# Performance work log

Hardware: AMD Instinct MI355X
Metric: run time of the kernel (lower is better)

Reference implementation:

```python
import jax, jax.numpy as jnp
import numpy as np

N_QUBITS = 14
N_LAYERS = 4
N_CLASSES = 10
BATCH = 1024


def apply_1q(state, gate, wire):
    """Apply a 2x2 gate ([2,2] shared or [B,2,2] batched) to `wire` of state [B,2,...,2]."""
    s = jnp.moveaxis(state, wire + 1, -1)
    shp = s.shape
    s = s.reshape(shp[0], -1, 2)
    if gate.ndim == 3:
        s = jnp.einsum('bij,bkj->bki', gate, s)
    else:
        s = jnp.einsum('ij,bkj->bki', gate, s)
    return jnp.moveaxis(s.reshape(shp), -1, wire + 1)


def apply_cnot(state, c, t):
    s = jnp.moveaxis(state, (c + 1, t + 1), (-2, -1))
    s = jnp.stack([s[..., 0, :], s[..., 1, ::-1]], axis=-2)
    return jnp.moveaxis(s, (-2, -1), (c + 1, t + 1))


def simulate(x, q_params):
    """Batched statevector sim of: RY(x_i) embed -> BasicEntanglerLayers(RX + CNOT ring) -> <Z_i>."""
    B, n = x.shape
    state = jnp.zeros((B,) + (2,) * n, jnp.complex64)
    state = state.at[(slice(None),) + (0,) * n].set(1.0)

    # RY(x_i) on each wire (angles batched per sample)
    c, s = jnp.cos(0.5 * x), jnp.sin(0.5 * x)
    for w in range(n):
        g = jnp.stack([jnp.stack([c[:, w], -s[:, w]], -1),
                       jnp.stack([s[:, w], c[:, w]], -1)], -2).astype(jnp.complex64)  # [B,2,2]
        state = apply_1q(state, g, w)

    # BasicEntanglerLayers: per layer RX(weights[l,i]) on every wire, then CNOT ring
    cw, sw = jnp.cos(0.5 * q_params), jnp.sin(0.5 * q_params)
    n_layers = q_params.shape[0]
    for l in range(n_layers):
        for w in range(n):
            cc = cw[l, w].astype(jnp.complex64)
            isw = (-1j) * sw[l, w].astype(jnp.complex64)
            g = jnp.stack([jnp.stack([cc, isw]), jnp.stack([isw, cc])])  # [2,2] RX
            state = apply_1q(state, g, w)
        if n == 2:
            state = apply_cnot(state, 0, 1)
        else:
            for w in range(n):
                state = apply_cnot(state, w, (w + 1) % n)

    # <Z_i> = P(bit_i=0) - P(bit_i=1)
    p = jnp.abs(state) ** 2  # [B,2,...,2] real
    axes_all = tuple(range(1, n + 1))
    z = []
    for w in range(n):
        pw = jnp.sum(p, axis=tuple(a for a in axes_all if a != w + 1))  # [B,2]
        z.append(pw[:, 0] - pw[:, 1])
    return jnp.stack(z, -1).astype(jnp.float32)  # [B, n]


def setup_inputs() -> dict:
    key = jax.random.key(0)
    k1, k2, k3, k4 = jax.random.split(key, 4)
    x = jax.random.normal(k1, (BATCH, N_QUBITS), dtype=jnp.float32)
    q_params = 0.01 * jax.random.normal(k2, (N_LAYERS, N_QUBITS), dtype=jnp.float32)
    fc_w = jax.random.normal(k3, (N_CLASSES, N_QUBITS), dtype=jnp.float32) / np.sqrt(N_QUBITS)
    fc_b = jax.random.normal(k4, (N_CLASSES,), dtype=jnp.float32) * 0.01
    return {"x": x, "q_params": q_params, "fc_w": fc_w, "fc_b": fc_b}


def reference(x, q_params, fc_w, fc_b):
    q_out = simulate(x, q_params)            # [B, n_qubits]
    logits = q_out @ fc_w.T + fc_b           # [B, n_classes]
    return logits
```

## Files before the change

kernel.cpp:

```cpp
#include <hip/hip_runtime.h>
#include <hip/hip_fp16.h>
#include <math.h>


#define NQ 14
#define NLAYERS 4
#define NCLASSES 10
#define BLOCK 512

typedef _Float16 f16;
typedef _Float16 f16x2 __attribute__((ext_vector_type(2)));
typedef _Float16 f16x4 __attribute__((ext_vector_type(4)));
typedef _Float16 f16x8 __attribute__((ext_vector_type(8)));
typedef float f32x4 __attribute__((ext_vector_type(4)));
typedef unsigned int u32;
typedef u32 u32x2 __attribute__((ext_vector_type(2)));

__device__ __forceinline__ f32x4 mf(f16x8 a, f16x8 b, f32x4 c) {
  return __builtin_amdgcn_mfma_f32_16x16x32_f16(a, b, c, 0, 0, 0);
}
__device__ __forceinline__ f32x4 mf16(f16x4 a, f16x4 b, f32x4 c) {
  return __builtin_amdgcn_mfma_f32_16x16x16f16(a, b, c, 0, 0, 0);
}
__device__ __forceinline__ int swz(int t) { return ((t ^ (t >> 3)) & 7) << 3; }

__device__ __forceinline__ f16x4 cvt4(f32x4 v) {
  u32x2 r;
  r[0] = __builtin_bit_cast(u32, __builtin_amdgcn_cvt_pkrtz(v[0], v[1]));
  r[1] = __builtin_bit_cast(u32, __builtin_amdgcn_cvt_pkrtz(v[2], v[3]));
  return __builtin_bit_cast(f16x4, r);
}
__device__ __forceinline__ u32 dwof(f16x4 v, int k) {
  return __builtin_bit_cast(u32x2, v)[k];
}

__device__ __forceinline__ int finv5(int n) {
  n ^= ((n >> 3) & 1) << 4;
  n ^= ((n >> 2) & 1) << 3;
  n ^= ((n >> 1) & 1) << 2;
  n ^= (n & 1) << 1;
  return n;
}
__device__ __forceinline__ int finv3(int n) {
  n ^= ((n >> 2) & 1) << 3;
  n ^= ((n >> 1) & 1) << 2;
  n ^= (n & 1) << 1;
  return n;
}

__global__ void qsim_build(const float* __restrict__ qp,
                           f16* __restrict__ gB, f16* __restrict__ gC) {
  __shared__ float qc[NLAYERS * NQ], qs[NLAYERS * NQ];
  const int tid = threadIdx.x;
  if (tid < NLAYERS * NQ) {
    float sv, cv; sincosf(0.5f * qp[tid], &sv, &cv);
    qc[tid] = cv; qs[tid] = sv;
  }
  __syncthreads();
#pragma unroll
  for (int p = 0; p < 7; ++p) {
    const int l = (p + 1) >> 1;
    const int base = 14 * l + ((p & 1) ? 0 : 5);
    const float c0 = qc[base], c1 = qc[base+1], c2 = qc[base+2], c3 = qc[base+3], c4 = qc[base+4];
    const float s0 = qs[base], s1 = qs[base+1], s2 = qs[base+2], s3 = qs[base+3], s4 = qs[base+4];
#pragma unroll
    for (int e = tid; e < 1024; e += BLOCK) {
      const int n = e >> 5, k = e & 31;
      const int d = finv5(n) ^ k;
      float mag = ((d & 1) ? s0 : c0) * ((d & 2) ? s1 : c1);
      mag *= ((d & 4) ? s2 : c2) * ((d & 8) ? s3 : c3);
      mag *= ((d & 16) ? s4 : c4);
      const int t = __popc(d) & 3;
      const f16 v = (f16)((t == 1 || t == 2) ? -mag : mag);
      const int pp = 256 * (k >> 3) + 8 * n + (k & 7);
      const bool isreal = !(t & 1);
      gB[p * 2048 + pp]        = isreal ? v : (f16)0.f;
      gB[p * 2048 + pp + 1024] = isreal ? (f16)0.f : v;
    }
  }
#pragma unroll
  for (int e = tid; e < 1024; e += BLOCK) {
    const int li = e >> 8, rp = (e >> 4) & 15, k = e & 15;
    const int base = 14 * li + 10;
    const float c0 = qc[base], c1 = qc[base+1], c2 = qc[base+2], c3 = qc[base+3];
    const float s0 = qs[base], s1 = qs[base+1], s2 = qs[base+2], s3 = qs[base+3];
    const int d = finv3(rp) ^ k;
    float mag = ((d & 1) ? s0 : c0) * ((d & 2) ? s1 : c1);
    mag *= ((d & 4) ? s2 : c2) * ((d & 8) ? s3 : c3);
    const int t = __popc(d) & 3;
    const f16 v = (f16)((t == 1 || t == 2) ? -mag : mag);
    const bool isreal = !(t & 1);
    const int pp = li * 512 + 16 * rp + k;
    gC[pp]       = isreal ? v : (f16)0.f;
    gC[pp + 256] = isreal ? (f16)0.f : v;
  }
}

struct FB { f16x8 br0, bi0, br1, bi1; };
struct FC { f16x4 ur0, ui0, ur1, ui1; };

__device__ __forceinline__ FB loadB(const f16* __restrict__ g, bool ctrl, int tid) {
  const int lane = tid & 63, wave = tid >> 6;
  const int q = lane >> 4, cc = lane & 15;
  int n0 = cc, n1 = cc | 16;
  if (ctrl && wave >= 4) { n0 ^= 31; n1 ^= 31; }
  FB f;
  f.br0 = *(const f16x8*)(g + 256 * q + 8 * n0);
  f.bi0 = *(const f16x8*)(g + 1024 + 256 * q + 8 * n0);
  f.br1 = *(const f16x8*)(g + 256 * q + 8 * n1);
  f.bi1 = *(const f16x8*)(g + 1024 + 256 * q + 8 * n1);
  return f;
}
__device__ __forceinline__ FC loadC(const f16* __restrict__ g, int tid) {
  const int lane = tid & 63;
  const int q = lane >> 4, cc = lane & 15;
  const int r0 = 16 * cc + 4 * q, r1 = 16 * (cc ^ 15) + 4 * q;
  FC f;
  f.ur0 = *(const f16x4*)(g + r0);
  f.ui0 = *(const f16x4*)(g + 256 + r0);
  f.ur1 = *(const f16x4*)(g + r1);
  f.ui1 = *(const f16x4*)(g + 256 + r1);
  return f;
}

__device__ __forceinline__ void passA(f16* __restrict__ reP, f16* __restrict__ imP,
                                      const FB fb,
                                      const f16* __restrict__ gNB,
                                      const f16* __restrict__ gNC,
                                      FB* __restrict__ nextB,
                                      FC* __restrict__ nextC, int tid) {
  const int lane = tid & 63, wave = tid >> 6;
  const int q = lane >> 4, cc = lane & 15;
  f16x8 Ar[4], Ai[4];
#pragma unroll
  for (int i = 0; i < 4; ++i) {
    const int mt = wave * 4 + i;
    const int pA = mt * 512 + ((128 * q + 8 * cc) ^ swz(mt));
    Ar[i] = *(const f16x8*)(reP + pA);
    Ai[i] = *(const f16x8*)(imP + pA);
  }
  __syncthreads();
  *nextB = loadB(gNB, true, tid);
  *nextC = loadC(gNC, tid);
  f16x4 outR[8], outI[8];
#pragma unroll
  for (int i = 0; i < 4; ++i) {
    const f16x8 nAi = -Ai[i];
    {
      f32x4 aR = {0.f,0.f,0.f,0.f}, aI = {0.f,0.f,0.f,0.f};
      aR = mf(Ar[i], fb.br0, aR); aR = mf(nAi, fb.bi0, aR);
      aI = mf(Ar[i], fb.bi0, aI); aI = mf(Ai[i], fb.br0, aI);
      outR[i * 2 + 0] = cvt4(aR);
      outI[i * 2 + 0] = cvt4(aI);
    }
    {
      f32x4 aR = {0.f,0.f,0.f,0.f}, aI = {0.f,0.f,0.f,0.f};
      aR = mf(Ar[i], fb.br1, aR); aR = mf(nAi, fb.bi1, aR);
      aI = mf(Ar[i], fb.bi1, aI); aI = mf(Ai[i], fb.br1, aI);
      outR[i * 2 + 1] = cvt4(aR);
      outI[i * 2 + 1] = cvt4(aI);
    }
  }
#pragma unroll
  for (int i = 0; i < 4; ++i) {
    const int mt = wave * 4 + i;
#pragma unroll
    for (int nt = 0; nt < 2; ++nt) {
      const int n5 = nt * 16 + cc;
      const int pS = n5 * 512 +
          ((128 * (2 * (mt & 1) + (q >> 1)) + 8 * (mt >> 1) + 4 * (q & 1)) ^ swz(n5));
      *(f16x4*)(reP + pS) = outR[i * 2 + nt];
      *(f16x4*)(imP + pS) = outI[i * 2 + nt];
    }
  }
}

template<bool FINAL>
__device__ __forceinline__ void superBC(f16* __restrict__ reP, f16* __restrict__ imP,
                                        const FB fb, const FC fc,
                                        const f16* __restrict__ gNB,
                                        FB* __restrict__ nextB,
                                        int tid, float* __restrict__ zloc) {
  const int lane = tid & 63, wave = tid >> 6;
  const int q = lane >> 4, cc = lane & 15;
  f16x8 Ar[4], Ai[4];
#pragma unroll
  for (int i = 0; i < 4; ++i) {
    const int mt = wave * 4 + i;
    const int pA = mt * 512 + ((128 * q + 8 * cc) ^ swz(mt));
    Ar[i] = *(const f16x8*)(reP + pA);
    Ai[i] = *(const f16x8*)(imP + pA);
  }
  if constexpr (!FINAL) {
    __syncthreads();
    *nextB = loadB(gNB, false, tid);
  }
  const f16x4 ucn0 = -fc.ui0, ucn1 = -fc.ui1;

  f16x4 accR[4][2], accI[4][2];
  float z0b = 0.f, z1b = 0.f, z9b = 0.f, zA = 0.f, zB = 0.f, pt = 0.f;
#pragma unroll
  for (int i = 0; i < 4; ++i) {
    const f16x8 nAi = -Ai[i];
#pragma unroll
    for (int h = 0; h < 2; ++h) {
      const f16x8 br = h ? fb.br1 : fb.br0;
      const f16x8 bi = h ? fb.bi1 : fb.bi0;
      f32x4 aR = {0.f,0.f,0.f,0.f}, aI = {0.f,0.f,0.f,0.f};
      aR = mf(Ar[i], br, aR); aR = mf(nAi, bi, aR);
      aI = mf(Ar[i], bi, aI); aI = mf(Ai[i], br, aI);
      const f16x4 s1r = cvt4(aR), s1i = cvt4(aI);
      const f16x4 ur = h ? fc.ur1 : fc.ur0;
      const f16x4 ui = h ? fc.ui1 : fc.ui0;
      const f16x4 un = h ? ucn1 : ucn0;
      f32x4 cR = {0.f,0.f,0.f,0.f}, cI = {0.f,0.f,0.f,0.f};
      cR = mf16(ur, s1r, cR); cR = mf16(un, s1i, cR);
      cI = mf16(ui, s1r, cI); cI = mf16(ur, s1i, cI);
      if constexpr (FINAL) {
        const float p0 = cR[0]*cR[0] + cI[0]*cI[0];
        const float p1 = cR[1]*cR[1] + cI[1]*cI[1];
        const float p2 = cR[2]*cR[2] + cI[2]*cI[2];
        const float p3 = cR[3]*cR[3] + cI[3]*cI[3];
        const float ps = (p0 + p1) + (p2 + p3);
        zA += (p0 - p1) + (p2 - p3);
        zB += (p0 + p1) - (p2 + p3);
        z0b += (i & 1) ? -ps : ps;
        z1b += (i & 2) ? -ps : ps;
        z9b += h ? -ps : ps;
        pt  += ps;
      } else {
        accR[i][h] = cvt4(cR);
        accI[i][h] = cvt4(cI);
      }
    }
  }
  if constexpr (FINAL) {
    zloc[0]  += (q & 2) ? -z0b : z0b;
    zloc[1]  += z1b;
    zloc[2]  += (wave & 1) ? -pt : pt;
    zloc[3]  += (wave & 2) ? -pt : pt;
    zloc[4]  += (wave & 4) ? -pt : pt;
    zloc[5]  += (cc & 1) ? -pt : pt;
    zloc[6]  += (cc & 2) ? -pt : pt;
    zloc[7]  += (cc & 4) ? -pt : pt;
    zloc[8]  += (cc & 8) ? -pt : pt;
    zloc[9]  += z9b;
    zloc[10] += zA;
    zloc[11] += zB;
    zloc[12] += (q & 1) ? -pt : pt;
    zloc[13] += (q & 2) ? -pt : pt;
  } else {
    const u32 selLo = (q & 2) ? 0x01000504u : 0x05040100u;
    const u32 selHi = (q & 2) ? 0x03020706u : 0x07060302u;
    const int ibase = 128 * (wave >> 1) + 4 * (wave & 1);
#pragma unroll
    for (int h = 0; h < 2; ++h) {
#pragma unroll
      for (int j = 0; j < 4; ++j) {
        const int pS = (8 * q + 2 * j + h) * 512 + ibase +
                       8 * (cc ^ (2 * j + h) ^ q);
        const int dj = j >> 1;
        const u32 sel = (j & 1) ? selHi : selLo;
        u32x2 vr, vi;
        vr[0] = __builtin_amdgcn_perm(dwof(accR[1][h], dj), dwof(accR[0][h], dj), sel);
        vr[1] = __builtin_amdgcn_perm(dwof(accR[3][h], dj), dwof(accR[2][h], dj), sel);
        vi[0] = __builtin_amdgcn_perm(dwof(accI[1][h], dj), dwof(accI[0][h], dj), sel);
        vi[1] = __builtin_amdgcn_perm(dwof(accI[3][h], dj), dwof(accI[2][h], dj), sel);
        *(u32x2*)(reP + pS) = vr;
        *(u32x2*)(imP + pS) = vi;
      }
    }
  }
}

__global__ __launch_bounds__(BLOCK, 4) void qsim_kernel(
    const float* __restrict__ x, const float* __restrict__ qp,
    const float* __restrict__ fcw, const float* __restrict__ fcb,
    const f16* __restrict__ gB, const f16* __restrict__ gC,
    float* __restrict__ out) {
  extern __shared__ unsigned char smem[];
  f16* reP = (f16*)smem;
  f16* imP = reP + 16384;
  float* scratch = (float*)(imP + 16384);
  float* qc = scratch + 128;
  float* qs = qc + 8;
  float* xc = qs + 8;
  float* xs = xc + 16;

  const int b = blockIdx.x;
  const int tid = threadIdx.x;

  FB fb = loadB(gB, true, tid);
  FC fc = loadC(gC, tid);

  if (tid < NQ) {
    float sv, cv; sincosf(0.5f * x[b * NQ + tid], &sv, &cv);
    xc[tid] = cv; xs[tid] = sv;
  } else if (tid >= 64 && tid < 64 + 5) {
    const int k = tid - 64;
    float sv, cv; sincosf(0.5f * qp[k], &sv, &cv);
    qc[k] = cv; qs[k] = sv;
  }
  __syncthreads();

  float* Flo  = scratch;
  float* psi  = Flo + 32;
  float* PsiR = psi + 32;
  float* PsiI = PsiR + 32;
  if (tid < 32) {
    float f = 1.f;
#pragma unroll
    for (int j = 0; j < 5; ++j) f *= ((tid >> j) & 1) ? xs[5 + j] : xc[5 + j];
    Flo[tid] = f;
  } else if (tid < 64) {
    const int k = tid - 32;
    float f = 1.f;
#pragma unroll
    for (int j = 0; j < 5; ++j) f *= ((k >> j) & 1) ? xs[j] : xc[j];
    psi[k] = f;
  }
  __syncthreads();
  if (tid < 32) {
    const float c0 = qc[0], c1 = qc[1], c2 = qc[2], c3 = qc[3], c4 = qc[4];
    const float s0 = qs[0], s1 = qs[1], s2 = qs[2], s3 = qs[3], s4 = qs[4];
    const int a = finv5(tid);
    float ar = 0.f, ai = 0.f;
    for (int k = 0; k < 32; ++k) {
      const int d = a ^ k;
      float mag = ((d & 1) ? s0 : c0) * ((d & 2) ? s1 : c1);
      mag *= ((d & 4) ? s2 : c2) * ((d & 8) ? s3 : c3);
      mag *= ((d & 16) ? s4 : c4);
      mag *= psi[k];
      const int t = __popc(d) & 3;
      if (t == 0) ar += mag; else if (t == 1) ai -= mag;
      else if (t == 2) ar -= mag; else ai += mag;
    }
    PsiR[tid] = ar; PsiI[tid] = ai;
  }
  __syncthreads();
  {
    float fhi = 1.f;
#pragma unroll
    for (int j = 0; j < 4; ++j) fhi *= ((tid >> j) & 1) ? xs[10 + j] : xc[10 + j];
    const float cr = fhi * PsiR[tid >> 4], ci = fhi * PsiI[tid >> 4];
    const int t = tid >> 4;
    const int sz = swz(t);
#pragma unroll
    for (int kb = 0; kb < 4; ++kb) {
      f16x8 hr, hi;
#pragma unroll
      for (int j = 0; j < 8; ++j) {
        const float F = Flo[8 * kb + j];
        hr[j] = (f16)(F * cr);
        hi[j] = (f16)(F * ci);
      }
      const int pb = t * 512 + ((128 * kb + 8 * (tid & 15)) ^ sz);
      *(f16x8*)(reP + pb) = hr;
      *(f16x8*)(imP + pb) = hi;
    }
  }
  __syncthreads();

  FB fbN; FC fcN;
  superBC<false>(reP, imP, fb, fc, gB + 1 * 2048, &fbN, tid, nullptr);
  __syncthreads();
#pragma unroll
  for (int l = 1; l < NLAYERS; ++l) {
    passA(reP, imP, fbN, gB + (2 * l) * 2048, gC + l * 512, &fb, &fc, tid);
    __syncthreads();
    if (l < NLAYERS - 1) {
      superBC<false>(reP, imP, fb, fc, gB + (2 * l + 1) * 2048, &fbN, tid, nullptr);
      __syncthreads();
    }
  }

  float zloc[NQ];
#pragma unroll
  for (int w = 0; w < NQ; ++w) zloc[w] = 0.f;
  superBC<true>(reP, imP, fb, fc, nullptr, nullptr, tid, zloc);
  __syncthreads();

  float* zpart = scratch;
  float* zbuf  = zpart + 112;
#pragma unroll
  for (int w = 0; w < NQ; ++w) {
#pragma unroll
    for (int off = 32; off > 0; off >>= 1)
      zloc[w] += __shfl_down(zloc[w], off, 64);
  }
  const int wave = tid >> 6, lane = tid & 63;
  if (lane == 0) {
#pragma unroll
    for (int w = 0; w < NQ; ++w) zpart[wave * NQ + w] = zloc[w];
  }
  __syncthreads();
  if (tid < NQ) {
    float a = 0.f;
#pragma unroll
    for (int v = 0; v < 8; ++v) a += zpart[v * NQ + tid];
    zbuf[tid] = a;
  }
  __syncthreads();
  if (tid < NCLASSES) {
    float acc = fcb[tid];
#pragma unroll
    for (int w = 0; w < NQ; ++w) acc = fmaf(zbuf[w], fcw[tid * NQ + w], acc);
    out[b * NCLASSES + tid] = acc;
  }
}

extern "C" void kernel_launch(void* const* d_in, const int* in_sizes, int n_in,
                              void* d_out, int out_size, void* d_ws, size_t ws_size,
                              hipStream_t stream) {
  const float* x   = (const float*)d_in[0];
  const float* qp  = (const float*)d_in[1];
  const float* fcw = (const float*)d_in[2];
  const float* fcb = (const float*)d_in[3];
  float* out = (float*)d_out;
  const int B = in_sizes[0] / NQ;

  f16* gB = (f16*)d_ws;
  f16* gC = gB + 7 * 2048;

  qsim_build<<<1, BLOCK, 0, stream>>>(qp, gB, gC);

  const size_t shmem = (size_t)(2 * 16384) * sizeof(f16)
                     + (size_t)(128 + 8 + 8 + 16 + 16) * sizeof(float);
  (void)hipFuncSetAttribute((const void*)qsim_kernel,
                            hipFuncAttributeMaxDynamicSharedMemorySize, (int)shmem);
  qsim_kernel<<<B, BLOCK, shmem, stream>>>(x, qp, fcw, fcb, gB, gC, out);
}
```

Before: 119.5 us.

## Halve LDS staging by exchanging real and imaginary parts sequentially through one buffer

The state is now held in registers between passes, and only one 32KB LDS staging buffer is used. Real and imaginary parts are transposed through it one after the other instead of keeping two full planes in shared memory. This halves the LDS footprint so more blocks fit per CU, and launch bounds rise from 4 to 6. In exchange each layer transition needs extra barriers and serialised LDS round trips, and register pressure under the tighter launch bound may cause spills.

After: 246.6 us. +106.3%, slower.

```diff
diff --git a/kernel.cpp b/kernel.cpp
--- a/kernel.cpp
+++ b/kernel.cpp
@@ -123,26 +123,80 @@
   return f;
 }
 
-__device__ __forceinline__ void passA(f16* __restrict__ reP, f16* __restrict__ imP,
-                                      const FB fb,
-                                      const f16* __restrict__ gNB,
-                                      const f16* __restrict__ gNC,
-                                      FB* __restrict__ nextB,
-                                      FC* __restrict__ nextC, int tid) {
+__device__ __forceinline__ void readFrag(const f16* __restrict__ stg, int tid,
+                                         f16x8 A[4]) {
   const int lane = tid & 63, wave = tid >> 6;
   const int q = lane >> 4, cc = lane & 15;
-  f16x8 Ar[4], Ai[4];
 #pragma unroll
   for (int i = 0; i < 4; ++i) {
     const int mt = wave * 4 + i;
-    const int pA = mt * 512 + ((128 * q + 8 * cc) ^ swz(mt));
-    Ar[i] = *(const f16x8*)(reP + pA);
-    Ai[i] = *(const f16x8*)(imP + pA);
-  }
-  __syncthreads();
-  *nextB = loadB(gNB, true, tid);
-  *nextC = loadC(gNC, tid);
-  f16x4 outR[8], outI[8];
+    A[i] = *(const f16x8*)(stg + mt * 512 + ((128 * q + 8 * cc) ^ swz(mt)));
+  }
+}
+__device__ __forceinline__ void storeA(f16* __restrict__ stg, int tid,
+                                       const f16x4 o[8]) {
+  const int lane = tid & 63, wave = tid >> 6;
+  const int q = lane >> 4, cc = lane & 15;
+#pragma unroll
+  for (int i = 0; i < 4; ++i) {
+    const int mt = wave * 4 + i;
+#pragma unroll
+    for (int nt = 0; nt < 2; ++nt) {
+      const int n5 = nt * 16 + cc;
+      const int pS = n5 * 512 +
+          ((128 * (2 * (mt & 1) + (q >> 1)) + 8 * (mt >> 1) + 4 * (q & 1)) ^ swz(n5));
+      *(f16x4*)(stg + pS) = o[i * 2 + nt];
+    }
+  }
+}
+__device__ __forceinline__ void storeBC(f16* __restrict__ stg, int tid,
+                                        const f16x4 a[4][2]) {
+  const int lane = tid & 63, wave = tid >> 6;
+  const int q = lane >> 4, cc = lane & 15;
+  const u32 selLo = (q & 2) ? 0x01000504u : 0x05040100u;
+  const u32 selHi = (q & 2) ? 0x03020706u : 0x07060302u;
+  const int ibase = 128 * (wave >> 1) + 4 * (wave & 1);
+#pragma unroll
+  for (int h = 0; h < 2; ++h) {
+#pragma unroll
+    for (int j = 0; j < 4; ++j) {
+      const int pS = (8 * q + 2 * j + h) * 512 + ibase + 8 * (cc ^ (2 * j + h) ^ q);
+      const int dj = j >> 1;
+      const u32 sel = (j & 1) ? selHi : selLo;
+      u32x2 v;
+      v[0] = __builtin_amdgcn_perm(dwof(a[1][h], dj), dwof(a[0][h], dj), sel);
+      v[1] = __builtin_amdgcn_perm(dwof(a[3][h], dj), dwof(a[2][h], dj), sel);
+      *(u32x2*)(stg + pS) = v;
+    }
+  }
+}
+__device__ __forceinline__ void exchangeA(f16* __restrict__ stg, int tid,
+                                          const f16x4 oR[8], const f16x4 oI[8],
+                                          f16x8 Ar[4], f16x8 Ai[4]) {
+  __syncthreads();
+  storeA(stg, tid, oR);
+  __syncthreads();
+  readFrag(stg, tid, Ar);
+  __syncthreads();
+  storeA(stg, tid, oI);
+  __syncthreads();
+  readFrag(stg, tid, Ai);
+}
+__device__ __forceinline__ void exchangeBC(f16* __restrict__ stg, int tid,
+                                           const f16x4 aR[4][2], const f16x4 aI[4][2],
+                                           f16x8 Ar[4], f16x8 Ai[4]) {
+  __syncthreads();
+  storeBC(stg, tid, aR);
+  __syncthreads();
+  readFrag(stg, tid, Ar);
+  __syncthreads();
+  storeBC(stg, tid, aI);
+  __syncthreads();
+  readFrag(stg, tid, Ai);
+}
+
+__device__ __forceinline__ void computeA(const f16x8 Ar[4], const f16x8 Ai[4],
+                                         const FB& fb, f16x4 oR[8], f16x4 oI[8]) {
 #pragma unroll
   for (int i = 0; i < 4; ++i) {
     const f16x8 nAi = -Ai[i];
@@ -150,54 +204,27 @@
       f32x4 aR = {0.f,0.f,0.f,0.f}, aI = {0.f,0.f,0.f,0.f};
       aR = mf(Ar[i], fb.br0, aR); aR = mf(nAi, fb.bi0, aR);
       aI = mf(Ar[i], fb.bi0, aI); aI = mf(Ai[i], fb.br0, aI);
-      outR[i * 2 + 0] = cvt4(aR);
-      outI[i * 2 + 0] = cvt4(aI);
+      oR[i * 2 + 0] = cvt4(aR);
+      oI[i * 2 + 0] = cvt4(aI);
     }
     {
       f32x4 aR = {0.f,0.f,0.f,0.f}, aI = {0.f,0.f,0.f,0.f};
       aR = mf(Ar[i], fb.br1, aR); aR = mf(nAi, fb.bi1, aR);
       aI = mf(Ar[i], fb.bi1, aI); aI = mf(Ai[i], fb.br1, aI);
-      outR[i * 2 + 1] = cvt4(aR);
-      outI[i * 2 + 1] = cvt4(aI);
-    }
-  }
-#pragma unroll
-  for (int i = 0; i < 4; ++i) {
-    const int mt = wave * 4 + i;
-#pragma unroll
-    for (int nt = 0; nt < 2; ++nt) {
-      const int n5 = nt * 16 + cc;
-      const int pS = n5 * 512 +
-          ((128 * (2 * (mt & 1) + (q >> 1)) + 8 * (mt >> 1) + 4 * (q & 1)) ^ swz(n5));
-      *(f16x4*)(reP + pS) = outR[i * 2 + nt];
-      *(f16x4*)(imP + pS) = outI[i * 2 + nt];
+      oR[i * 2 + 1] = cvt4(aR);
+      oI[i * 2 + 1] = cvt4(aI);
     }
   }
 }
 
 template<bool FINAL>
-__device__ __forceinline__ void superBC(f16* __restrict__ reP, f16* __restrict__ imP,
-                                        const FB fb, const FC fc,
-                                        const f16* __restrict__ gNB,
-                                        FB* __restrict__ nextB,
-                                        int tid, float* __restrict__ zloc) {
+__device__ __forceinline__ void computeBC(const f16x8 Ar[4], const f16x8 Ai[4],
+                                          const FB& fb, const FC& fc,
+                                          f16x4 aR4[4][2], f16x4 aI4[4][2],
+                                          int tid, float* __restrict__ zloc) {
   const int lane = tid & 63, wave = tid >> 6;
   const int q = lane >> 4, cc = lane & 15;
-  f16x8 Ar[4], Ai[4];
-#pragma unroll
-  for (int i = 0; i < 4; ++i) {
-    const int mt = wave * 4 + i;
-    const int pA = mt * 512 + ((128 * q + 8 * cc) ^ swz(mt));
-    Ar[i] = *(const f16x8*)(reP + pA);
-    Ai[i] = *(const f16x8*)(imP + pA);
-  }
-  if constexpr (!FINAL) {
-    __syncthreads();
-    *nextB = loadB(gNB, false, tid);
-  }
   const f16x4 ucn0 = -fc.ui0, ucn1 = -fc.ui1;
-
-  f16x4 accR[4][2], accI[4][2];
   float z0b = 0.f, z1b = 0.f, z9b = 0.f, zA = 0.f, zB = 0.f, pt = 0.f;
 #pragma unroll
   for (int i = 0; i < 4; ++i) {
@@ -229,8 +256,8 @@
         z9b += h ? -ps : ps;
         pt  += ps;
       } else {
-        accR[i][h] = cvt4(cR);
-        accI[i][h] = cvt4(cI);
+        aR4[i][h] = cvt4(cR);
+        aI4[i][h] = cvt4(cI);
       }
     }
   }
@@ -249,39 +276,17 @@
     zloc[11] += zB;
     zloc[12] += (q & 1) ? -pt : pt;
     zloc[13] += (q & 2) ? -pt : pt;
-  } else {
-    const u32 selLo = (q & 2) ? 0x01000504u : 0x05040100u;
-    const u32 selHi = (q & 2) ? 0x03020706u : 0x07060302u;
-    const int ibase = 128 * (wave >> 1) + 4 * (wave & 1);
-#pragma unroll
-    for (int h = 0; h < 2; ++h) {
-#pragma unroll
-      for (int j = 0; j < 4; ++j) {
-        const int pS = (8 * q + 2 * j + h) * 512 + ibase +
-                       8 * (cc ^ (2 * j + h) ^ q);
-        const int dj = j >> 1;
-        const u32 sel = (j & 1) ? selHi : selLo;
-        u32x2 vr, vi;
-        vr[0] = __builtin_amdgcn_perm(dwof(accR[1][h], dj), dwof(accR[0][h], dj), sel);
-        vr[1] = __builtin_amdgcn_perm(dwof(accR[3][h], dj), dwof(accR[2][h], dj), sel);
-        vi[0] = __builtin_amdgcn_perm(dwof(accI[1][h], dj), dwof(accI[0][h], dj), sel);
-        vi[1] = __builtin_amdgcn_perm(dwof(accI[3][h], dj), dwof(accI[2][h], dj), sel);
-        *(u32x2*)(reP + pS) = vr;
-        *(u32x2*)(imP + pS) = vi;
-      }
-    }
-  }
-}
-
-__global__ __launch_bounds__(BLOCK, 4) void qsim_kernel(
+  }
+}
+
+__global__ __launch_bounds__(BLOCK, 6) void qsim_kernel(
     const float* __restrict__ x, const float* __restrict__ qp,
     const float* __restrict__ fcw, const float* __restrict__ fcb,
     const f16* __restrict__ gB, const f16* __restrict__ gC,
     float* __restrict__ out) {
   extern __shared__ unsigned char smem[];
-  f16* reP = (f16*)smem;
-  f16* imP = reP + 16384;
-  float* scratch = (float*)(imP + 16384);
+  f16* stg = (f16*)smem;
+  float* scratch = (float*)(stg + 16384);
   float* qc = scratch + 128;
   float* qs = qc + 8;
   float* xc = qs + 8;
@@ -338,6 +343,8 @@
     PsiR[tid] = ar; PsiI[tid] = ai;
   }
   __syncthreads();
+
+  f16x8 Ar[4], Ai[4];
   {
     float fhi = 1.f;
 #pragma unroll
@@ -347,37 +354,60 @@
     const int sz = swz(t);
 #pragma unroll
     for (int kb = 0; kb < 4; ++kb) {
-      f16x8 hr, hi;
-#pragma unroll
-      for (int j = 0; j < 8; ++j) {
-        const float F = Flo[8 * kb + j];
-        hr[j] = (f16)(F * cr);
-        hi[j] = (f16)(F * ci);
-      }
-      const int pb = t * 512 + ((128 * kb + 8 * (tid & 15)) ^ sz);
-      *(f16x8*)(reP + pb) = hr;
-      *(f16x8*)(imP + pb) = hi;
-    }
-  }
-  __syncthreads();
-
-  FB fbN; FC fcN;
-  superBC<false>(reP, imP, fb, fc, gB + 1 * 2048, &fbN, tid, nullptr);
-  __syncthreads();
-#pragma unroll
-  for (int l = 1; l < NLAYERS; ++l) {
-    passA(reP, imP, fbN, gB + (2 * l) * 2048, gC + l * 512, &fb, &fc, tid);
+      f16x8 hr;
+#pragma unroll
+      for (int j = 0; j < 8; ++j) hr[j] = (f16)(Flo[8 * kb + j] * cr);
+      *(f16x8*)(stg + t * 512 + ((128 * kb + 8 * (tid & 15)) ^ sz)) = hr;
+    }
     __syncthreads();
-    if (l < NLAYERS - 1) {
-      superBC<false>(reP, imP, fb, fc, gB + (2 * l + 1) * 2048, &fbN, tid, nullptr);
-      __syncthreads();
-    }
-  }
+    readFrag(stg, tid, Ar);
+    __syncthreads();
+#pragma unroll
+    for (int kb = 0; kb < 4; ++kb) {
+      f16x8 hi;
+#pragma unroll
+      for (int j = 0; j < 8; ++j) hi[j] = (f16)(Flo[8 * kb + j] * ci);
+      *(f16x8*)(stg + t * 512 + ((128 * kb + 8 * (tid & 15)) ^ sz)) = hi;
+    }
+    __syncthreads();
+    readFrag(stg, tid, Ai);
+  }
+
+  f16x4 aR4[4][2], aI4[4][2];
+  f16x4 oR[8], oI[8];
+  FB fbA, fbB; FC fcB;
+
+  fbA = loadB(gB + 1 * 2048, false, tid);
+  computeBC<false>(Ar, Ai, fb, fc, aR4, aI4, tid, nullptr);
+  exchangeBC(stg, tid, aR4, aI4, Ar, Ai);
+
+  fbB = loadB(gB + 2 * 2048, true, tid);
+  fcB = loadC(gC + 1 * 512, tid);
+  computeA(Ar, Ai, fbA, oR, oI);
+  exchangeA(stg, tid, oR, oI, Ar, Ai);
+
+  fbA = loadB(gB + 3 * 2048, false, tid);
+  computeBC<false>(Ar, Ai, fbB, fcB, aR4, aI4, tid, nullptr);
+  exchangeBC(stg, tid, aR4, aI4, Ar, Ai);
+
+  fbB = loadB(gB + 4 * 2048, true, tid);
+  fcB = loadC(gC + 2 * 512, tid);
+  computeA(Ar, Ai, fbA, oR, oI);
+  exchangeA(stg, tid, oR, oI, Ar, Ai);
+
+  fbA = loadB(gB + 5 * 2048, false, tid);
+  computeBC<false>(Ar, Ai, fbB, fcB, aR4, aI4, tid, nullptr);
+  exchangeBC(stg, tid, aR4, aI4, Ar, Ai);
+
+  fbB = loadB(gB + 6 * 2048, true, tid);
+  fcB = loadC(gC + 3 * 512, tid);
+  computeA(Ar, Ai, fbA, oR, oI);
+  exchangeA(stg, tid, oR, oI, Ar, Ai);
 
   float zloc[NQ];
 #pragma unroll
   for (int w = 0; w < NQ; ++w) zloc[w] = 0.f;
-  superBC<true>(reP, imP, fb, fc, nullptr, nullptr, tid, zloc);
+  computeBC<true>(Ar, Ai, fbB, fcB, aR4, aI4, tid, zloc);
   __syncthreads();
 
   float* zpart = scratch;
@@ -424,7 +454,7 @@
 
   qsim_build<<<1, BLOCK, 0, stream>>>(qp, gB, gC);
 
-  const size_t shmem = (size_t)(2 * 16384) * sizeof(f16)
+  const size_t shmem = (size_t)16384 * sizeof(f16)
                      + (size_t)(128 + 8 + 8 + 16 + 16) * sizeof(float);
   (void)hipFuncSetAttribute((const void*)qsim_kernel,
                             hipFuncAttributeMaxDynamicSharedMemorySize, (int)shmem);
```
